# Kernel tuning notes

Hardware: AMD Instinct MI355X
Metric: run time of the kernel (lower is better)

Reference implementation:

```python
import jax, jax.numpy as jnp
import numpy as np

N = 50000      # nodes per type
E = 800000     # edges per type (avg degree 16)
D = 128        # feature dim == hidden_channels
L = 3          # num_layers
G = 16         # graphs in batch
OUT = 2


def setup_inputs() -> dict:
    key = jax.random.key(0)
    ks = jax.random.split(key, 12)
    return {
        "x_void": jax.random.normal(ks[0], (N, D), jnp.float32),
        "x_vessel": jax.random.normal(ks[1], (N, D), jnp.float32),
        "Wl": jax.random.normal(ks[2], (L, 2, D, D), jnp.float32) * 0.05,
        "bl": jax.random.normal(ks[3], (L, 2, D), jnp.float32) * 0.05,
        "Wr": jax.random.normal(ks[4], (L, 2, D, D), jnp.float32) * 0.05,
        "lin_W": jax.random.normal(ks[5], (2 * D, OUT), jnp.float32) * 0.05,
        "lin_b": jax.random.normal(ks[6], (OUT,), jnp.float32) * 0.05,
        "edge_void": jax.random.randint(ks[7], (2, E), 0, N, jnp.int64 if jax.config.jax_enable_x64 else jnp.int32),
        "edge_vessel": jax.random.randint(ks[8], (2, E), 0, N, jnp.int64 if jax.config.jax_enable_x64 else jnp.int32),
        "batch_void": jnp.sort(jax.random.randint(ks[9], (N,), 0, G)),
        "batch_vessel": jnp.sort(jax.random.randint(ks[10], (N,), 0, G)),
    }


def _sage(x, src, dst, Wl_t, bl_t, Wr_t):
    # PyG SAGEConv (aggr='mean'): lin_l(mean_{j in N(i)} x_j) + lin_r(x_i)
    n = x.shape[0]
    agg = jax.ops.segment_sum(x[src], dst, num_segments=n)  # [n, D]
    cnt = jax.ops.segment_sum(jnp.ones((src.shape[0],), x.dtype), dst, num_segments=n)
    mean = agg / jnp.maximum(cnt, 1.0)[:, None]
    return mean @ Wl_t + bl_t + x @ Wr_t


def _mean_pool(x, batch, num_graphs):
    s = jax.ops.segment_sum(x, batch, num_segments=num_graphs)
    c = jax.ops.segment_sum(jnp.ones((x.shape[0],), x.dtype), batch, num_segments=num_graphs)
    return s / jnp.maximum(c, 1.0)[:, None]


def reference(x_void, x_vessel, Wl, bl, Wr, lin_W, lin_b,
              edge_void, edge_vessel, batch_void, batch_vessel):
    xs = [x_void, x_vessel]
    edges = [edge_void, edge_vessel]
    for l in range(L):
        xs = [jax.nn.relu(_sage(xs[t], edges[t][0], edges[t][1], Wl[l, t], bl[l, t], Wr[l, t]))
              for t in range(2)]
    reps = [_mean_pool(xs[0], batch_void, G), _mean_pool(xs[1], batch_vessel, G)]
    h = jnp.concatenate(reps, axis=1)  # [G, 2D]; dropout inactive (training=False)
    return h @ lin_W + lin_b
```

## Files before the change

kernel.cpp:

```cpp
#include <hip/hip_runtime.h>
#include <hip/hip_bf16.h>
#include <cstdint>
#include <cstddef>

static constexpr int FD = 128;
static constexpr int NG = 16;
static constexpr int NL = 3;

typedef __attribute__((ext_vector_type(8))) short short8;
typedef __attribute__((ext_vector_type(4))) float floatx4;

__device__ __forceinline__ short f2bf(float v) {
  union { __hip_bfloat16 b; short s; } u;
  u.b = __float2bfloat16(v);
  return u.s;
}
__device__ __forceinline__ float bfu(unsigned short u) {
  return __uint_as_float((unsigned int)u << 16);
}

__global__ __launch_bounds__(256) void k_bucket(
    const int* __restrict__ e0, const int* __restrict__ e1,
    int* __restrict__ gcount, int* __restrict__ buckets,
    int E, int NBUCK, int CAP)
{
  __shared__ int hist[256], lexcl[256], gbase[256], wcur[256];
  __shared__ int staged[4096];
  __shared__ int wsum[4];
  __shared__ int totalS;
  int tid = (int)threadIdx.x;
  int bx = (int)blockIdx.x;
  int t = bx & 1;
  int chunk = (bx >> 1) * 4096;
  const int* eg = t ? e1 : e0;
  hist[tid] = 0;
  __syncthreads();
  unsigned int ent[16];
  #pragma unroll
  for (int k = 0; k < 16; k++) {
    int i = chunk + k * 256 + tid;
    if (i < E) {
      unsigned int src = (unsigned int)eg[i];
      unsigned int dst = (unsigned int)eg[E + i];
      ent[k] = src | (dst << 16);
      atomicAdd(&hist[dst >> 8], 1);
    } else ent[k] = 0xFFFFFFFFu;
  }
  __syncthreads();
  int lane = tid & 63, wv = tid >> 6;
  int v = hist[tid];
  int sc = v;
  #pragma unroll
  for (int d = 1; d < 64; d <<= 1) {
    int tt = __shfl_up(sc, d, 64);
    if (lane >= d) sc += tt;
  }
  if (lane == 63) wsum[wv] = sc;
  __syncthreads();
  int wpre = 0;
  for (int w = 0; w < wv; w++) wpre += wsum[w];
  int excl = wpre + sc - v;
  lexcl[tid] = excl;
  wcur[tid] = excl;
  gbase[tid] = v ? atomicAdd(&gcount[t * 256 + tid], v) : 0;
  if (tid == 255) totalS = excl + v;
  __syncthreads();
  #pragma unroll
  for (int k = 0; k < 16; k++) {
    if (ent[k] != 0xFFFFFFFFu) {
      int b = ent[k] >> 24;
      int pos = atomicAdd(&wcur[b], 1);
      staged[pos] = (int)ent[k];
    }
  }
  __syncthreads();
  int total = totalS;
  for (int j = tid; j < total; j += 256) {
    unsigned int e = (unsigned int)staged[j];
    int b = e >> 24;
    int gp = gbase[b] + (j - lexcl[b]);
    if (gp < CAP) buckets[((size_t)t * NBUCK + b) * CAP + gp] = (int)e;
  }
}

__global__ __launch_bounds__(256) void k_csr(
    const int* __restrict__ gcount, const int* __restrict__ buckets,
    unsigned short* __restrict__ csr0, unsigned short* __restrict__ csr1,
    int* __restrict__ off0, int* __restrict__ off1,
    int* __restrict__ deg0, int* __restrict__ deg1,
    int NBUCK, int CAP, int n)
{
  __shared__ int hist[256], wcur[256], wsum[4];
  int tid = (int)threadIdx.x;
  int bx = (int)blockIdx.x;
  int t = bx & 1;
  int b = bx >> 1;
  int cnt = gcount[t * 256 + b];
  if (cnt > CAP) cnt = CAP;
  const int* base = buckets + ((size_t)t * NBUCK + b) * CAP;
  unsigned short* csr = t ? csr1 : csr0;
  int* off = t ? off1 : off0;
  int* deg = t ? deg1 : deg0;
  hist[tid] = 0;
  __syncthreads();
  for (int j = tid; j < cnt; j += 256)
    atomicAdd(&hist[((unsigned int)base[j] >> 16) & 255], 1);
  __syncthreads();
  int lane = tid & 63, wv = tid >> 6;
  int v = hist[tid];
  int sc = v;
  #pragma unroll
  for (int d = 1; d < 64; d <<= 1) {
    int tt = __shfl_up(sc, d, 64);
    if (lane >= d) sc += tt;
  }
  if (lane == 63) wsum[wv] = sc;
  __syncthreads();
  int wpre = 0;
  for (int w = 0; w < wv; w++) wpre += wsum[w];
  int excl = wpre + sc - v;
  wcur[tid] = excl;
  int node = b * 256 + tid;
  if (node < n) { deg[node] = v; off[node] = b * CAP + excl; }
  __syncthreads();
  for (int j = tid; j < cnt; j += 256) {
    unsigned int e = (unsigned int)base[j];
    int ld = (e >> 16) & 255;
    int pos = atomicAdd(&wcur[ld], 1);
    csr[b * CAP + pos] = (unsigned short)(e & 0xFFFFu);
  }
}

__global__ void k_wconv(const float* __restrict__ Wl, const float* __restrict__ Wr,
                        short* __restrict__ Wf) {
  int u = blockIdx.x * blockDim.x + threadIdx.x;
  if (u >= 6 * 8192) return;
  int combo = u >> 13;
  int r = u & 8191;
  int l  = r & 63;
  int nt = (r >> 6) & 7;
  int h  = (r >> 9) & 1;
  int ks = r >> 10;
  short8 s;
  #pragma unroll
  for (int j = 0; j < 8; j++) {
    int k = ks * 32 + (l >> 4) * 8 + j;
    int n = nt * 16 + (l & 15);
    float w = (k < FD) ? Wl[((size_t)combo * FD + k) * FD + n]
                       : Wr[((size_t)combo * FD + (k - FD)) * FD + n];
    __hip_bfloat16 hb = __float2bfloat16(w);
    if (h == 0) {
      union { __hip_bfloat16 b; short t; } uu; uu.b = hb; s[j] = uu.t;
    } else {
      float hf = __bfloat162float(hb);
      s[j] = f2bf(w - hf);
    }
  }
  *(short8*)(Wf + (size_t)combo * 65536 + (size_t)r * 8) = s;
}

__global__ __launch_bounds__(256) void k_xconv(
    const float* __restrict__ x0, const float* __restrict__ x1,
    short* __restrict__ a0, short* __restrict__ a1,
    short* __restrict__ r0, short* __restrict__ r1, int n) {
  int bx = blockIdx.x;
  int t = bx & 1;
  int g = bx >> 1;
  const float* x = t ? x1 : x0;
  short* a = t ? a1 : a0;
  short* rm = t ? r1 : r0;
  int tid = (int)threadIdx.x;
  int m = tid & 15;
  int kb = tid >> 4;
  int node = g * 16 + m;
  if (node >= n) return;
  const float* src = x + (size_t)node * FD + kb * 8;
  short8 s;
  #pragma unroll
  for (int j = 0; j < 8; j++) s[j] = f2bf(src[j]);
  *(short8*)(a + (size_t)g * 2048 + kb * 128 + m * 8) = s;
  *(short8*)(rm + (size_t)node * FD + kb * 8) = s;
}

__global__ __launch_bounds__(512) void k_agg(
    const unsigned short* __restrict__ x0, const unsigned short* __restrict__ x1,
    const unsigned short* __restrict__ csr0, const unsigned short* __restrict__ csr1,
    const int* __restrict__ off0, const int* __restrict__ off1,
    const int* __restrict__ deg0, const int* __restrict__ deg1,
    short* __restrict__ m0, short* __restrict__ m1, int n)
{
  __shared__ float M[16][132];
  int bx = blockIdx.x;
  int t = bx & 1;
  int g = bx >> 1;
  const unsigned short* x = t ? x1 : x0;
  const unsigned short* csr = t ? csr1 : csr0;
  const int* off  = t ? off1 : off0;
  const int* deg  = t ? deg1 : deg0;
  short* mAF      = t ? m1 : m0;
  int tid = (int)threadIdx.x;
  int s = tid >> 5;
  int tx = tid & 31;
  int c4 = tx * 4;
  int node = g * 16 + s;
  if (node < n) {
    int o = off[node], d = deg[node];
    float a0 = 0.f, a1 = 0.f, a2 = 0.f, a3 = 0.f;
    for (int k0 = 0; k0 < d; k0 += 32) {
      int idx = (k0 + tx < d) ? (int)csr[o + k0 + tx] : 0;
      int mm = min(32, d - k0);
      int j = 0;
      for (; j + 8 <= mm; j += 8) {
        int s0 = __shfl(idx, j + 0, 32);
        int s1 = __shfl(idx, j + 1, 32);
        int s2 = __shfl(idx, j + 2, 32);
        int s3 = __shfl(idx, j + 3, 32);
        int s4 = __shfl(idx, j + 4, 32);
        int s5 = __shfl(idx, j + 5, 32);
        int s6 = __shfl(idx, j + 6, 32);
        int s7 = __shfl(idx, j + 7, 32);
        ushort4 u0 = *(const ushort4*)&x[(size_t)s0 * FD + c4];
        ushort4 u1 = *(const ushort4*)&x[(size_t)s1 * FD + c4];
        ushort4 u2 = *(const ushort4*)&x[(size_t)s2 * FD + c4];
        ushort4 u3 = *(const ushort4*)&x[(size_t)s3 * FD + c4];
        ushort4 u4 = *(const ushort4*)&x[(size_t)s4 * FD + c4];
        ushort4 u5 = *(const ushort4*)&x[(size_t)s5 * FD + c4];
        ushort4 u6 = *(const ushort4*)&x[(size_t)s6 * FD + c4];
        ushort4 u7 = *(const ushort4*)&x[(size_t)s7 * FD + c4];
        a0 += ((bfu(u0.x) + bfu(u1.x)) + (bfu(u2.x) + bfu(u3.x)))
            + ((bfu(u4.x) + bfu(u5.x)) + (bfu(u6.x) + bfu(u7.x)));
        a1 += ((bfu(u0.y) + bfu(u1.y)) + (bfu(u2.y) + bfu(u3.y)))
            + ((bfu(u4.y) + bfu(u5.y)) + (bfu(u6.y) + bfu(u7.y)));
        a2 += ((bfu(u0.z) + bfu(u1.z)) + (bfu(u2.z) + bfu(u3.z)))
            + ((bfu(u4.z) + bfu(u5.z)) + (bfu(u6.z) + bfu(u7.z)));
        a3 += ((bfu(u0.w) + bfu(u1.w)) + (bfu(u2.w) + bfu(u3.w)))
            + ((bfu(u4.w) + bfu(u5.w)) + (bfu(u6.w) + bfu(u7.w)));
      }
      for (; j < mm; j++) {
        int si = __shfl(idx, j, 32);
        ushort4 u = *(const ushort4*)&x[(size_t)si * FD + c4];
        a0 += bfu(u.x); a1 += bfu(u.y); a2 += bfu(u.z); a3 += bfu(u.w);
      }
    }
    float inv = 1.f / fmaxf((float)d, 1.f);
    M[s][c4 + 0] = a0 * inv;
    M[s][c4 + 1] = a1 * inv;
    M[s][c4 + 2] = a2 * inv;
    M[s][c4 + 3] = a3 * inv;
  }
  __syncthreads();
  if (tid < 256) {
    int m = tid & 15;
    int kb = tid >> 4;
    if (g * 16 + m < n) {
      short8 v;
      #pragma unroll
      for (int j = 0; j < 8; j++) v[j] = f2bf(M[m][kb * 8 + j]);
      *(short8*)(mAF + (size_t)g * 2048 + kb * 128 + m * 8) = v;
    }
  }
}

__global__ __launch_bounds__(256) void k_gemm(
    const short* __restrict__ mAF0, const short* __restrict__ mAF1,
    const short* __restrict__ xAF0, const short* __restrict__ xAF1,
    const short* __restrict__ Wf,
    const float* __restrict__ bl,
    short* __restrict__ obf0, short* __restrict__ obf1,
    short* __restrict__ oAF0, short* __restrict__ oAF1, int n)
{
  __shared__ __align__(16) char smem[32768];
  short* WfL = (short*)smem;
  float* S   = (float*)smem;

  int tid = (int)threadIdx.x;
  int l = tid & 63;
  int wv = tid >> 6;
  int bx = (int)blockIdx.x;
  int t = bx & 1;
  int tile = bx >> 1;
  int row0 = tile * 128;
  int g0 = tile * 8;

  const short* mAF = t ? mAF1 : mAF0;
  const short* xAF = t ? xAF1 : xAF0;
  const short* Wc  = Wf + (size_t)t * 65536;
  const float* bias = bl + t * FD;
  short* obf = t ? obf1 : obf0;
  short* oAF = t ? oAF1 : oAF0;

  int rhalf = wv & 1;
  int chalf = wv >> 1;
  int laneoff = (l >> 4) * 128 + (l & 15) * 8;

  auto stageW = [&](int ks, int buf) {
    const short* src = Wc + ks * 8192 + wv * 2048;
    short* dst = WfL + buf * 8192 + wv * 2048;
    #pragma unroll
    for (int i = 0; i < 4; i++) {
      __builtin_amdgcn_global_load_lds(
          (const __attribute__((address_space(1))) void*)(src + i * 512 + l * 8),
          (__attribute__((address_space(3))) void*)(dst + i * 512),
          16, 0, 0);
    }
  };

  floatx4 acc[4][4];
  #pragma unroll
  for (int i = 0; i < 4; i++)
    #pragma unroll
    for (int q = 0; q < 4; q++) acc[i][q] = (floatx4)0.f;

  short8 Acur[4], Anext[4];
  auto loadA = [&](int ks, short8* A) {
    const short* Ab = (ks < 4 ? mAF : xAF) + (ks & 3) * 512;
    #pragma unroll
    for (int i = 0; i < 4; i++) {
      int g = g0 + rhalf * 4 + i;
      A[i] = *(const short8*)(Ab + (size_t)g * 2048 + laneoff);
    }
  };

  stageW(0, 0);
  loadA(0, Acur);
  for (int ks = 0; ks < 8; ks++) {
    int buf = ks & 1;
    __syncthreads();
    if (ks < 7) { stageW(ks + 1, buf ^ 1); loadA(ks + 1, Anext); }
    const short* WB = WfL + buf * 8192;
    #pragma unroll
    for (int q = 0; q < 4; q++) {
      int nt = chalf * 4 + q;
      short8 whi = *(const short8*)(WB + nt * 512 + l * 8);
      short8 wlo = *(const short8*)(WB + 4096 + nt * 512 + l * 8);
      #pragma unroll
      for (int i = 0; i < 4; i++) {
        acc[i][q] = __builtin_amdgcn_mfma_f32_16x16x32_bf16(Acur[i], whi, acc[i][q], 0, 0, 0);
        acc[i][q] = __builtin_amdgcn_mfma_f32_16x16x32_bf16(Acur[i], wlo, acc[i][q], 0, 0, 0);
      }
    }
    #pragma unroll
    for (int i = 0; i < 4; i++) Acur[i] = Anext[i];
  }

  #pragma unroll
  for (int q = 0; q < 4; q++) {
    int col = chalf * 64 + q * 16 + (l & 15);
    float b = bias[col];
    #pragma unroll
    for (int i = 0; i < 4; i++)
      #pragma unroll
      for (int r = 0; r < 4; r++)
        acc[i][q][r] = fmaxf(acc[i][q][r] + b, 0.f);
  }

  #pragma unroll
  for (int ph = 0; ph < 2; ph++) {
    __syncthreads();
    if (chalf == ph) {
      #pragma unroll
      for (int i = 0; i < 4; i++)
        #pragma unroll
        for (int q = 0; q < 4; q++)
          #pragma unroll
          for (int r = 0; r < 4; r++)
            S[(rhalf * 64 + i * 16 + (l >> 4) * 4 + r) * 64 + q * 16 + (l & 15)] = acc[i][q][r];
    }
    __syncthreads();
    #pragma unroll
    for (int it = 0; it < 4; it++) {
      int u = it * 256 + tid;
      int m = u & 15;
      int kb = (u >> 4) & 7;
      int grp = u >> 7;
      int rl = grp * 16 + m;
      if (row0 + rl < n) {
        short8 s;
        #pragma unroll
        for (int j = 0; j < 8; j++) s[j] = f2bf(S[rl * 64 + kb * 8 + j]);
        *(short8*)(oAF + (size_t)(g0 + grp) * 2048 + (ph * 8 + kb) * 128 + m * 8) = s;
        *(short8*)(obf + (size_t)(row0 + rl) * FD + ph * 64 + kb * 8) = s;
      }
    }
  }
}

__global__ __launch_bounds__(256) void k_pool1(
    const unsigned short* __restrict__ x0, const unsigned short* __restrict__ x1,
    const int* __restrict__ b0, const int* __restrict__ b1,
    float* __restrict__ part, int n, int NCH) {
  __shared__ float R[8][128];
  __shared__ int sb;
  int bx = (int)blockIdx.x;
  int t = bx & 1;
  int ch = bx >> 1;
  const unsigned short* x = t ? x1 : x0;
  const int* batch = t ? b1 : b0;
  float* P = part + ((size_t)t * NCH + ch) * 272;
  int tid = (int)threadIdx.x;
  int tx = tid & 31, rs = tid >> 5;
  int c4 = tx * 4;
  int start = ch * 128;
  int end = min(start + 128, n);

  int g0 = batch[start];
  int g1 = batch[end - 1];
  int lo[2], hi[2];
  int nruns;
  if (g0 == g1) {
    lo[0] = start; hi[0] = end; nruns = 1;
  } else {
    if (tid == 0) sb = end;
    __syncthreads();
    for (int i = start + tid + 1; i < end; i += 256)
      if (batch[i] != batch[i - 1]) atomicMin(&sb, i);
    __syncthreads();
    int b = sb;
    lo[0] = start; hi[0] = b; lo[1] = b; hi[1] = end; nruns = 2;
  }

  for (int run = 0; run < nruns; run++) {
    float4 a = make_float4(0.f, 0.f, 0.f, 0.f);
    for (int i = lo[run] + rs; i < hi[run]; i += 8) {
      ushort4 u = *(const ushort4*)&x[(size_t)i * FD + c4];
      a.x += bfu(u.x); a.y += bfu(u.y); a.z += bfu(u.z); a.w += bfu(u.w);
    }
    *(float4*)&R[rs][c4] = a;
    __syncthreads();
    if (tid < 128) {
      float s = 0.f;
      #pragma unroll
      for (int r = 0; r < 8; r++) s += R[r][tid];
      P[run * 128 + tid] = s;
    }
    __syncthreads();
  }
  if (tid == 0) {
    P[256] = (float)g0;
    P[257] = (float)(hi[0] - lo[0]);
    P[258] = (nruns == 2) ? (float)g1 : -1.f;
    P[259] = (nruns == 2) ? (float)(hi[1] - lo[1]) : 0.f;
  }
}

__global__ __launch_bounds__(128) void k_pool2(
    const float* __restrict__ part, float* __restrict__ pool,
    float* __restrict__ pcnt, int NCH, int CPS) {
  int bx = (int)blockIdx.x;
  int t = bx & 1;
  int seg = bx >> 1;
  int c0 = seg * CPS;
  int c1 = min(c0 + CPS, NCH);
  int tid = (int)threadIdx.x;
  float* pl = pool + t * NG * FD;
  float* pc = pcnt + t * NG;
  float acc = 0.f, ccnt = 0.f;
  int curg = -1;
  for (int ch = c0; ch < c1; ch++) {
    const float* P = part + ((size_t)t * NCH + ch) * 272;
    #pragma unroll
    for (int r = 0; r < 2; r++) {
      int g = (int)P[256 + r * 2];
      if (g < 0) continue;
      if (g != curg) {
        if (curg >= 0) {
          atomicAdd(&pl[curg * FD + tid], acc);
          if (tid == 0) atomicAdd(&pc[curg], ccnt);
        }
        curg = g; acc = 0.f; ccnt = 0.f;
      }
      acc += P[r * 128 + tid];
      if (tid == 0) ccnt += P[257 + r * 2];
    }
  }
  if (curg >= 0) {
    atomicAdd(&pl[curg * FD + tid], acc);
    if (tid == 0) atomicAdd(&pc[curg], ccnt);
  }
}

__global__ void k_final(const float* __restrict__ pool, const float* __restrict__ pcnt,
                        const float* __restrict__ linW, const float* __restrict__ linb,
                        float* __restrict__ out) {
  int tid = (int)threadIdx.x;
  if (tid < NG * 2) {
    int g = tid >> 1, o = tid & 1;
    float s = linb[o];
    for (int t = 0; t < 2; t++) {
      float inv = 1.f / fmaxf(pcnt[t * NG + g], 1.f);
      for (int d = 0; d < FD; d++) {
        float h = pool[(t * NG + g) * FD + d] * inv;
        s = fmaf(h, linW[(t * FD + d) * 2 + o], s);
      }
    }
    out[g * 2 + o] = s;
  }
}

extern "C" void kernel_launch(void* const* d_in, const int* in_sizes, int n_in,
                              void* d_out, int out_size, void* d_ws, size_t ws_size,
                              hipStream_t stream) {
  const float* x_in[2] = {(const float*)d_in[0], (const float*)d_in[1]};
  const float* Wl   = (const float*)d_in[2];
  const float* bl   = (const float*)d_in[3];
  const float* Wr   = (const float*)d_in[4];
  const float* linW = (const float*)d_in[5];
  const float* linb = (const float*)d_in[6];
  const int* edges[2] = {(const int*)d_in[7], (const int*)d_in[8]};
  const int* batch[2] = {(const int*)d_in[9], (const int*)d_in[10]};

  const int N = in_sizes[0] / FD;
  const int E = in_sizes[7] / 2;
  const int NGRP = (N + 15) / 16;
  const int NTILE = (N + 127) / 128;
  const int NCH = (N + 127) / 128;
  const int NBUCK = (N + 255) / 256;
  const int CAP = 5120;
  const size_t AFG = (size_t)(NTILE * 8 + 8) * 2048;

  char* p = (char*)d_ws;
  auto alloc = [&](size_t bytes) -> char* {
    char* r = p; p += (bytes + 511) & ~(size_t)511; return r;
  };
  int* gcount  = (int*)alloc(2 * 256 * 4);
  float* pool  = (float*)alloc(2 * NG * FD * 4);
  float* pcnt  = (float*)alloc(2 * NG * 4);
  size_t zero_bytes = (size_t)(p - (char*)d_ws);
  int* off[2];  off[0]  = (int*)alloc((size_t)N * 4); off[1]  = (int*)alloc((size_t)N * 4);
  int* deg[2];  deg[0]  = (int*)alloc((size_t)N * 4); deg[1]  = (int*)alloc((size_t)N * 4);
  int* buckets = (int*)alloc((size_t)2 * NBUCK * CAP * 4);
  unsigned short* csr[2];
  csr[0] = (unsigned short*)alloc((size_t)NBUCK * CAP * 2);
  csr[1] = (unsigned short*)alloc((size_t)NBUCK * CAP * 2);
  float* part  = (float*)alloc((size_t)2 * NCH * 272 * 4);
  short* Wf    = (short*)alloc((size_t)6 * 65536 * 2);
  short* mAF[2]; mAF[0] = (short*)alloc(AFG * 2); mAF[1] = (short*)alloc(AFG * 2);
  short* xAF[2][2];
  for (int t = 0; t < 2; t++)
    for (int b = 0; b < 2; b++) xAF[t][b] = (short*)alloc(AFG * 2);
  short* xbf[2][2];
  for (int t = 0; t < 2; t++)
    for (int b = 0; b < 2; b++) xbf[t][b] = (short*)alloc((size_t)N * FD * 2);
  if ((size_t)(p - (char*)d_ws) > ws_size) return;

  hipMemsetAsync(d_ws, 0, zero_bytes, stream);

  k_wconv<<<(6 * 8192 + 255) / 256, 256, 0, stream>>>(Wl, Wr, Wf);
  k_xconv<<<2 * NGRP, 256, 0, stream>>>(x_in[0], x_in[1],
                                        xAF[0][0], xAF[1][0], xbf[0][0], xbf[1][0], N);
  int bblocks = 2 * ((E + 4095) / 4096);
  k_bucket<<<bblocks, 256, 0, stream>>>(edges[0], edges[1], gcount, buckets, E, NBUCK, CAP);
  k_csr<<<2 * NBUCK, 256, 0, stream>>>(gcount, buckets, csr[0], csr[1],
                                       off[0], off[1], deg[0], deg[1], NBUCK, CAP, N);

  int pp = 0;
  for (int l = 0; l < NL; l++) {
    k_agg<<<2 * NGRP, 512, 0, stream>>>(
        (const unsigned short*)xbf[0][pp], (const unsigned short*)xbf[1][pp],
        csr[0], csr[1], off[0], off[1], deg[0], deg[1], mAF[0], mAF[1], N);
    k_gemm<<<2 * NTILE, 256, 0, stream>>>(
        mAF[0], mAF[1], xAF[0][pp], xAF[1][pp],
        Wf + (size_t)l * 2 * 65536, bl + (size_t)l * 2 * FD,
        xbf[0][pp ^ 1], xbf[1][pp ^ 1], xAF[0][pp ^ 1], xAF[1][pp ^ 1], N);
    pp ^= 1;
  }

  k_pool1<<<2 * NCH, 256, 0, stream>>>(
      (const unsigned short*)xbf[0][pp], (const unsigned short*)xbf[1][pp],
      batch[0], batch[1], part, N, NCH);
  int CPS = (NCH + 7) / 8;
  k_pool2<<<16, 128, 0, stream>>>(part, pool, pcnt, NCH, CPS);
  k_final<<<1, 64, 0, stream>>>(pool, pcnt, linW, linb, (float*)d_out);
}
```

Baseline: 447.8 us.

## Shrink aggregation blocks, deepen gather unroll, skip unused last-layer fragment store

The aggregation kernel now uses 256-thread blocks covering 8 nodes instead of 512-thread blocks covering 16. This doubles the block count for finer scheduling and better load balance across CUs. The neighbour gather loop now issues 16 independent loads before accumulating, to raise memory-level parallelism. The last layer's GEMM also skips writing the MFMA-layout copy, which nothing reads. The trade-offs are higher register pressure from the deeper unroll and a changed floating-point summation order.

```diff
diff --git a/kernel.cpp b/kernel.cpp
--- a/kernel.cpp
+++ b/kernel.cpp
@@ -182,27 +182,27 @@
   *(short8*)(rm + (size_t)node * FD + kb * 8) = s;
 }
 
-__global__ __launch_bounds__(512) void k_agg(
+__global__ __launch_bounds__(256) void k_agg(
     const unsigned short* __restrict__ x0, const unsigned short* __restrict__ x1,
     const unsigned short* __restrict__ csr0, const unsigned short* __restrict__ csr1,
     const int* __restrict__ off0, const int* __restrict__ off1,
     const int* __restrict__ deg0, const int* __restrict__ deg1,
     short* __restrict__ m0, short* __restrict__ m1, int n)
 {
-  __shared__ float M[16][132];
-  int bx = blockIdx.x;
-  int t = bx & 1;
-  int g = bx >> 1;
+  __shared__ float M[8][132];
+  int bx = (int)blockIdx.x;
+  int t = bx & 1;
+  int blk = bx >> 1;
   const unsigned short* x = t ? x1 : x0;
   const unsigned short* csr = t ? csr1 : csr0;
-  const int* off  = t ? off1 : off0;
-  const int* deg  = t ? deg1 : deg0;
-  short* mAF      = t ? m1 : m0;
+  const int* off = t ? off1 : off0;
+  const int* deg = t ? deg1 : deg0;
+  short* mAF = t ? m1 : m0;
   int tid = (int)threadIdx.x;
   int s = tid >> 5;
   int tx = tid & 31;
   int c4 = tx * 4;
-  int node = g * 16 + s;
+  int node = blk * 8 + s;
   if (node < n) {
     int o = off[node], d = deg[node];
     float a0 = 0.f, a1 = 0.f, a2 = 0.f, a3 = 0.f;
@@ -210,31 +210,31 @@
       int idx = (k0 + tx < d) ? (int)csr[o + k0 + tx] : 0;
       int mm = min(32, d - k0);
       int j = 0;
+      for (; j + 16 <= mm; j += 16) {
+        ushort4 u[16];
+        #pragma unroll
+        for (int q = 0; q < 16; q++) {
+          int si = __shfl(idx, j + q, 32);
+          u[q] = *(const ushort4*)&x[(size_t)si * FD + c4];
+        }
+        #pragma unroll
+        for (int q = 0; q < 16; q++) {
+          a0 += bfu(u[q].x); a1 += bfu(u[q].y);
+          a2 += bfu(u[q].z); a3 += bfu(u[q].w);
+        }
+      }
       for (; j + 8 <= mm; j += 8) {
-        int s0 = __shfl(idx, j + 0, 32);
-        int s1 = __shfl(idx, j + 1, 32);
-        int s2 = __shfl(idx, j + 2, 32);
-        int s3 = __shfl(idx, j + 3, 32);
-        int s4 = __shfl(idx, j + 4, 32);
-        int s5 = __shfl(idx, j + 5, 32);
-        int s6 = __shfl(idx, j + 6, 32);
-        int s7 = __shfl(idx, j + 7, 32);
-        ushort4 u0 = *(const ushort4*)&x[(size_t)s0 * FD + c4];
-        ushort4 u1 = *(const ushort4*)&x[(size_t)s1 * FD + c4];
-        ushort4 u2 = *(const ushort4*)&x[(size_t)s2 * FD + c4];
-        ushort4 u3 = *(const ushort4*)&x[(size_t)s3 * FD + c4];
-        ushort4 u4 = *(const ushort4*)&x[(size_t)s4 * FD + c4];
-        ushort4 u5 = *(const ushort4*)&x[(size_t)s5 * FD + c4];
-        ushort4 u6 = *(const ushort4*)&x[(size_t)s6 * FD + c4];
-        ushort4 u7 = *(const ushort4*)&x[(size_t)s7 * FD + c4];
-        a0 += ((bfu(u0.x) + bfu(u1.x)) + (bfu(u2.x) + bfu(u3.x)))
-            + ((bfu(u4.x) + bfu(u5.x)) + (bfu(u6.x) + bfu(u7.x)));
-        a1 += ((bfu(u0.y) + bfu(u1.y)) + (bfu(u2.y) + bfu(u3.y)))
-            + ((bfu(u4.y) + bfu(u5.y)) + (bfu(u6.y) + bfu(u7.y)));
-        a2 += ((bfu(u0.z) + bfu(u1.z)) + (bfu(u2.z) + bfu(u3.z)))
-            + ((bfu(u4.z) + bfu(u5.z)) + (bfu(u6.z) + bfu(u7.z)));
-        a3 += ((bfu(u0.w) + bfu(u1.w)) + (bfu(u2.w) + bfu(u3.w)))
-            + ((bfu(u4.w) + bfu(u5.w)) + (bfu(u6.w) + bfu(u7.w)));
+        ushort4 u[8];
+        #pragma unroll
+        for (int q = 0; q < 8; q++) {
+          int si = __shfl(idx, j + q, 32);
+          u[q] = *(const ushort4*)&x[(size_t)si * FD + c4];
+        }
+        #pragma unroll
+        for (int q = 0; q < 8; q++) {
+          a0 += bfu(u[q].x); a1 += bfu(u[q].y);
+          a2 += bfu(u[q].z); a3 += bfu(u[q].w);
+        }
       }
       for (; j < mm; j++) {
         int si = __shfl(idx, j, 32);
@@ -249,13 +249,16 @@
     M[s][c4 + 3] = a3 * inv;
   }
   __syncthreads();
-  if (tid < 256) {
-    int m = tid & 15;
-    int kb = tid >> 4;
-    if (g * 16 + m < n) {
+  if (tid < 128) {
+    int st = tid >> 4;
+    int kb = tid & 15;
+    int nd = blk * 8 + st;
+    if (nd < n) {
+      int g = nd >> 4;
+      int m = nd & 15;
       short8 v;
       #pragma unroll
-      for (int j = 0; j < 8; j++) v[j] = f2bf(M[m][kb * 8 + j]);
+      for (int jj = 0; jj < 8; jj++) v[jj] = f2bf(M[st][kb * 8 + jj]);
       *(short8*)(mAF + (size_t)g * 2048 + kb * 128 + m * 8) = v;
     }
   }
@@ -267,7 +270,7 @@
     const short* __restrict__ Wf,
     const float* __restrict__ bl,
     short* __restrict__ obf0, short* __restrict__ obf1,
-    short* __restrict__ oAF0, short* __restrict__ oAF1, int n)
+    short* __restrict__ oAF0, short* __restrict__ oAF1, int n, int last)
 {
   __shared__ __align__(16) char smem[32768];
   short* WfL = (short*)smem;
@@ -378,7 +381,8 @@
         short8 s;
         #pragma unroll
         for (int j = 0; j < 8; j++) s[j] = f2bf(S[rl * 64 + kb * 8 + j]);
-        *(short8*)(oAF + (size_t)(g0 + grp) * 2048 + (ph * 8 + kb) * 128 + m * 8) = s;
+        if (!last)
+          *(short8*)(oAF + (size_t)(g0 + grp) * 2048 + (ph * 8 + kb) * 128 + m * 8) = s;
         *(short8*)(obf + (size_t)(row0 + rl) * FD + ph * 64 + kb * 8) = s;
       }
     }
@@ -554,14 +558,16 @@
                                        off[0], off[1], deg[0], deg[1], NBUCK, CAP, N);
 
   int pp = 0;
+  int ablocks = 2 * ((N + 7) / 8);
   for (int l = 0; l < NL; l++) {
-    k_agg<<<2 * NGRP, 512, 0, stream>>>(
+    k_agg<<<ablocks, 256, 0, stream>>>(
         (const unsigned short*)xbf[0][pp], (const unsigned short*)xbf[1][pp],
         csr[0], csr[1], off[0], off[1], deg[0], deg[1], mAF[0], mAF[1], N);
     k_gemm<<<2 * NTILE, 256, 0, stream>>>(
         mAF[0], mAF[1], xAF[0][pp], xAF[1][pp],
         Wf + (size_t)l * 2 * 65536, bl + (size_t)l * 2 * FD,
-        xbf[0][pp ^ 1], xbf[1][pp ^ 1], xAF[0][pp ^ 1], xAF[1][pp ^ 1], N);
+        xbf[0][pp ^ 1], xbf[1][pp ^ 1], xAF[0][pp ^ 1], xAF[1][pp ^ 1], N,
+        (l == NL - 1) ? 1 : 0);
     pp ^= 1;
   }
 
```

New measurement: 490.9 us. 9.6% more time.

## Drop MFMA-fragment activation copies and read A directly from row-major bf16

Applied to the files above, without the earlier changes.

The GEMM now loads its A operand straight from the row-major bf16 node buffers (mean and previous features) instead of from separate MFMA-fragment-ordered copies. This removes the duplicate fragment-layout writes in the conversion, aggregation and GEMM epilogue kernels, along with their buffers. The weight and input conversion kernels are merged into one launch. The A loads become strided row reads with 256-byte stride, which may coalesce less well than the old contiguous fragment reads. Buffers are padded to whole tiles so the reads stay in bounds.

```diff
diff --git a/kernel.cpp b/kernel.cpp
--- a/kernel.cpp
+++ b/kernel.cpp
@@ -131,55 +131,53 @@
   }
 }
 
-__global__ void k_wconv(const float* __restrict__ Wl, const float* __restrict__ Wr,
-                        short* __restrict__ Wf) {
-  int u = blockIdx.x * blockDim.x + threadIdx.x;
-  if (u >= 6 * 8192) return;
-  int combo = u >> 13;
-  int r = u & 8191;
-  int l  = r & 63;
-  int nt = (r >> 6) & 7;
-  int h  = (r >> 9) & 1;
-  int ks = r >> 10;
-  short8 s;
-  #pragma unroll
-  for (int j = 0; j < 8; j++) {
-    int k = ks * 32 + (l >> 4) * 8 + j;
-    int n = nt * 16 + (l & 15);
-    float w = (k < FD) ? Wl[((size_t)combo * FD + k) * FD + n]
-                       : Wr[((size_t)combo * FD + (k - FD)) * FD + n];
-    __hip_bfloat16 hb = __float2bfloat16(w);
-    if (h == 0) {
-      union { __hip_bfloat16 b; short t; } uu; uu.b = hb; s[j] = uu.t;
-    } else {
-      float hf = __bfloat162float(hb);
-      s[j] = f2bf(w - hf);
-    }
-  }
-  *(short8*)(Wf + (size_t)combo * 65536 + (size_t)r * 8) = s;
-}
-
-__global__ __launch_bounds__(256) void k_xconv(
+__global__ __launch_bounds__(256) void k_conv(
+    const float* __restrict__ Wl, const float* __restrict__ Wr,
+    short* __restrict__ Wf,
     const float* __restrict__ x0, const float* __restrict__ x1,
-    short* __restrict__ a0, short* __restrict__ a1,
     short* __restrict__ r0, short* __restrict__ r1, int n) {
-  int bx = blockIdx.x;
-  int t = bx & 1;
-  int g = bx >> 1;
-  const float* x = t ? x1 : x0;
-  short* a = t ? a1 : a0;
-  short* rm = t ? r1 : r0;
-  int tid = (int)threadIdx.x;
-  int m = tid & 15;
-  int kb = tid >> 4;
-  int node = g * 16 + m;
-  if (node >= n) return;
-  const float* src = x + (size_t)node * FD + kb * 8;
-  short8 s;
-  #pragma unroll
-  for (int j = 0; j < 8; j++) s[j] = f2bf(src[j]);
-  *(short8*)(a + (size_t)g * 2048 + kb * 128 + m * 8) = s;
-  *(short8*)(rm + (size_t)node * FD + kb * 8) = s;
+  int bx = (int)blockIdx.x;
+  int tid = (int)threadIdx.x;
+  if (bx < 192) {
+    int u = bx * 256 + tid;
+    int combo = u >> 13;
+    int r = u & 8191;
+    int l  = r & 63;
+    int nt = (r >> 6) & 7;
+    int h  = (r >> 9) & 1;
+    int ks = r >> 10;
+    short8 s;
+    #pragma unroll
+    for (int j = 0; j < 8; j++) {
+      int k = ks * 32 + (l >> 4) * 8 + j;
+      int nn = nt * 16 + (l & 15);
+      float w = (k < FD) ? Wl[((size_t)combo * FD + k) * FD + nn]
+                         : Wr[((size_t)combo * FD + (k - FD)) * FD + nn];
+      __hip_bfloat16 hb = __float2bfloat16(w);
+      if (h == 0) {
+        union { __hip_bfloat16 b; short t; } uu; uu.b = hb; s[j] = uu.t;
+      } else {
+        float hf = __bfloat162float(hb);
+        s[j] = f2bf(w - hf);
+      }
+    }
+    *(short8*)(Wf + (size_t)combo * 65536 + (size_t)r * 8) = s;
+  } else {
+    int b2 = bx - 192;
+    int t = b2 & 1;
+    int g = b2 >> 1;
+    const float* x = t ? x1 : x0;
+    short* rm = t ? r1 : r0;
+    int m = tid & 15;
+    int kb = tid >> 4;
+    int node = g * 16 + m;
+    if (node >= n) return;
+    const float* src = x + (size_t)node * FD + kb * 8;
+    short8 s;
+    #pragma unroll
+    for (int j = 0; j < 8; j++) s[j] = f2bf(src[j]);
+    *(short8*)(rm + (size_t)node * FD + kb * 8) = s;
+  }
 }
 
 __global__ __launch_bounds__(512) void k_agg(
@@ -197,7 +195,7 @@
   const unsigned short* csr = t ? csr1 : csr0;
   const int* off  = t ? off1 : off0;
   const int* deg  = t ? deg1 : deg0;
-  short* mAF      = t ? m1 : m0;
+  short* mrm      = t ? m1 : m0;
   int tid = (int)threadIdx.x;
   int s = tid >> 5;
   int tx = tid & 31;
@@ -252,22 +250,22 @@
   if (tid < 256) {
     int m = tid & 15;
     int kb = tid >> 4;
-    if (g * 16 + m < n) {
+    int nd = g * 16 + m;
+    if (nd < n) {
       short8 v;
       #pragma unroll
       for (int j = 0; j < 8; j++) v[j] = f2bf(M[m][kb * 8 + j]);
-      *(short8*)(mAF + (size_t)g * 2048 + kb * 128 + m * 8) = v;
+      *(short8*)(mrm + (size_t)nd * FD + kb * 8) = v;
     }
   }
 }
 
 __global__ __launch_bounds__(256) void k_gemm(
-    const short* __restrict__ mAF0, const short* __restrict__ mAF1,
-    const short* __restrict__ xAF0, const short* __restrict__ xAF1,
+    const unsigned short* __restrict__ mrm0, const unsigned short* __restrict__ mrm1,
+    const unsigned short* __restrict__ xin0, const unsigned short* __restrict__ xin1,
     const short* __restrict__ Wf,
     const float* __restrict__ bl,
-    short* __restrict__ obf0, short* __restrict__ obf1,
-    short* __restrict__ oAF0, short* __restrict__ oAF1, int n)
+    short* __restrict__ obf0, short* __restrict__ obf1, int n)
 {
   __shared__ __align__(16) char smem[32768];
   short* WfL = (short*)smem;
@@ -280,18 +278,15 @@
   int t = bx & 1;
   int tile = bx >> 1;
   int row0 = tile * 128;
-  int g0 = tile * 8;
-
-  const short* mAF = t ? mAF1 : mAF0;
-  const short* xAF = t ? xAF1 : xAF0;
+
+  const unsigned short* mrm = t ? mrm1 : mrm0;
+  const unsigned short* xin = t ? xin1 : xin0;
   const short* Wc  = Wf + (size_t)t * 65536;
   const float* bias = bl + t * FD;
   short* obf = t ? obf1 : obf0;
-  short* oAF = t ? oAF1 : oAF0;
 
   int rhalf = wv & 1;
   int chalf = wv >> 1;
-  int laneoff = (l >> 4) * 128 + (l & 15) * 8;
 
   auto stageW = [&](int ks, int buf) {
     const short* src = Wc + ks * 8192 + wv * 2048;
@@ -313,12 +308,12 @@
 
   short8 Acur[4], Anext[4];
   auto loadA = [&](int ks, short8* A) {
-    const short* Ab = (ks < 4 ? mAF : xAF) + (ks & 3) * 512;
-    #pragma unroll
-    for (int i = 0; i < 4; i++) {
-      int g = g0 + rhalf * 4 + i;
-      A[i] = *(const short8*)(Ab + (size_t)g * 2048 + laneoff);
-    }
+    const unsigned short* Ab = (ks < 4) ? mrm : xin;
+    int fo = (ks & 3) * 32 + (l >> 4) * 8;
+    int ndb = row0 + rhalf * 64 + (l & 15);
+    #pragma unroll
+    for (int i = 0; i < 4; i++)
+      A[i] = *(const short8*)(Ab + (size_t)(ndb + i * 16) * FD + fo);
   };
 
   stageW(0, 0);
@@ -378,7 +373,6 @@
         short8 s;
         #pragma unroll
         for (int j = 0; j < 8; j++) s[j] = f2bf(S[rl * 64 + kb * 8 + j]);
-        *(short8*)(oAF + (size_t)(g0 + grp) * 2048 + (ph * 8 + kb) * 128 + m * 8) = s;
         *(short8*)(obf + (size_t)(row0 + rl) * FD + ph * 64 + kb * 8) = s;
       }
     }
@@ -516,7 +510,7 @@
   const int NCH = (N + 127) / 128;
   const int NBUCK = (N + 255) / 256;
   const int CAP = 5120;
-  const size_t AFG = (size_t)(NTILE * 8 + 8) * 2048;
+  const int NPAD = NTILE * 128;
 
   char* p = (char*)d_ws;
   auto alloc = [&](size_t bytes) -> char* {
@@ -534,20 +528,18 @@
   csr[1] = (unsigned short*)alloc((size_t)NBUCK * CAP * 2);
   float* part  = (float*)alloc((size_t)2 * NCH * 272 * 4);
   short* Wf    = (short*)alloc((size_t)6 * 65536 * 2);
-  short* mAF[2]; mAF[0] = (short*)alloc(AFG * 2); mAF[1] = (short*)alloc(AFG * 2);
-  short* xAF[2][2];
-  for (int t = 0; t < 2; t++)
-    for (int b = 0; b < 2; b++) xAF[t][b] = (short*)alloc(AFG * 2);
+  short* meanb[2];
+  meanb[0] = (short*)alloc((size_t)NPAD * FD * 2);
+  meanb[1] = (short*)alloc((size_t)NPAD * FD * 2);
   short* xbf[2][2];
   for (int t = 0; t < 2; t++)
-    for (int b = 0; b < 2; b++) xbf[t][b] = (short*)alloc((size_t)N * FD * 2);
+    for (int b = 0; b < 2; b++) xbf[t][b] = (short*)alloc((size_t)NPAD * FD * 2);
   if ((size_t)(p - (char*)d_ws) > ws_size) return;
 
   hipMemsetAsync(d_ws, 0, zero_bytes, stream);
 
-  k_wconv<<<(6 * 8192 + 255) / 256, 256, 0, stream>>>(Wl, Wr, Wf);
-  k_xconv<<<2 * NGRP, 256, 0, stream>>>(x_in[0], x_in[1],
-                                        xAF[0][0], xAF[1][0], xbf[0][0], xbf[1][0], N);
+  k_conv<<<192 + 2 * NGRP, 256, 0, stream>>>(Wl, Wr, Wf, x_in[0], x_in[1],
+                                             xbf[0][0], xbf[1][0], N);
   int bblocks = 2 * ((E + 4095) / 4096);
   k_bucket<<<bblocks, 256, 0, stream>>>(edges[0], edges[1], gcount, buckets, E, NBUCK, CAP);
   k_csr<<<2 * NBUCK, 256, 0, stream>>>(gcount, buckets, csr[0], csr[1],
@@ -557,11 +549,12 @@
   for (int l = 0; l < NL; l++) {
     k_agg<<<2 * NGRP, 512, 0, stream>>>(
         (const unsigned short*)xbf[0][pp], (const unsigned short*)xbf[1][pp],
-        csr[0], csr[1], off[0], off[1], deg[0], deg[1], mAF[0], mAF[1], N);
+        csr[0], csr[1], off[0], off[1], deg[0], deg[1], meanb[0], meanb[1], N);
     k_gemm<<<2 * NTILE, 256, 0, stream>>>(
-        mAF[0], mAF[1], xAF[0][pp], xAF[1][pp],
+        (const unsigned short*)meanb[0], (const unsigned short*)meanb[1],
+        (const unsigned short*)xbf[0][pp], (const unsigned short*)xbf[1][pp],
         Wf + (size_t)l * 2 * 65536, bl + (size_t)l * 2 * FD,
-        xbf[0][pp ^ 1], xbf[1][pp ^ 1], xAF[0][pp ^ 1], xAF[1][pp ^ 1], N);
+        xbf[0][pp ^ 1], xbf[1][pp ^ 1], N);
     pp ^= 1;
   }
 
```

New measurement: 458.0 us. 1.02x slower.
